# Kernel optimization log

Measured on AMD Instinct MI355X. Metric: run time of the kernel, lower is better.

Reference implementation:

```python
import jax, jax.numpy as jnp
import numpy as np

N, M, N0 = 100000, 12, 2500            # atoms, max neighbors, crystals
ORIG, C, NBR, H, NCONV = 92, 64, 41, 128, 3
EPS = 1e-5                              # torch BatchNorm1d default eps


def setup_inputs() -> dict:
    key = jax.random.key(0)
    ks = jax.random.split(key, 10)
    return {
        "atom_fea": jax.random.normal(ks[0], (N, ORIG), jnp.float32),
        "nbr_fea": jax.random.normal(ks[1], (N, M, NBR), jnp.float32),
        "nbr_fea_idx": jax.random.randint(ks[2], (N, M), 0, N),
        "crystal_atom_idx": jnp.sort(jax.random.randint(ks[3], (N,), 0, N0)),
        # learned parameters (Linear weights stored as (in, out))
        "emb_W": jax.random.normal(ks[4], (ORIG, C), jnp.float32) * 0.05,
        "emb_b": jnp.zeros((C,), jnp.float32),
        "fc_W": jax.random.normal(ks[5], (NCONV, 2 * C + NBR, 2 * C), jnp.float32) * 0.05,
        "fc_b": jnp.zeros((NCONV, 2 * C), jnp.float32),
        "bn1_g": jnp.ones((NCONV, 2 * C), jnp.float32),
        "bn1_b": jnp.zeros((NCONV, 2 * C), jnp.float32),
        "bn2_g": jnp.ones((NCONV, C), jnp.float32),
        "bn2_b": jnp.zeros((NCONV, C), jnp.float32),
        "head_W": jax.random.normal(ks[6], (C, H), jnp.float32) * 0.05,
        "head_b": jnp.zeros((H,), jnp.float32),
        "out_W": jax.random.normal(ks[7], (H, 1), jnp.float32) * 0.05,
        "out_b": jnp.zeros((1,), jnp.float32),
    }


def _bn(x, g, b):
    # training-mode BatchNorm1d: per-feature batch mean/var (biased)
    mu = jnp.mean(x, axis=0)
    var = jnp.var(x, axis=0)
    return (x - mu) * jax.lax.rsqrt(var + EPS) * g + b


def reference(atom_fea, nbr_fea, nbr_fea_idx, crystal_atom_idx,
              emb_W, emb_b, fc_W, fc_b, bn1_g, bn1_b, bn2_g, bn2_b,
              head_W, head_b, out_W, out_b):
    h = atom_fea @ emb_W + emb_b                       # (N, C)
    for l in range(NCONV):
        nbr_h = h[nbr_fea_idx]                         # gather (N, M, C)
        self_h = jnp.broadcast_to(h[:, None, :], (N, M, C))
        tot = jnp.concatenate([self_h, nbr_h, nbr_fea], axis=2)  # (N, M, 2C+NBR)
        g = tot @ fc_W[l] + fc_b[l]                    # (N, M, 2C)
        g = _bn(g.reshape(-1, 2 * C), bn1_g[l], bn1_b[l]).reshape(N, M, 2 * C)
        filt = jax.nn.sigmoid(g[..., :C])
        core = jax.nn.softplus(g[..., C:])
        summed = jnp.sum(filt * core, axis=1)          # (N, C)
        summed = _bn(summed, bn2_g[l], bn2_b[l])
        h = jax.nn.softplus(h + summed)                # residual
    # per-crystal mean pooling via segment sum
    counts = jax.ops.segment_sum(jnp.ones((N,), h.dtype), crystal_atom_idx, num_segments=N0)
    crys = jax.ops.segment_sum(h, crystal_atom_idx, num_segments=N0) / jnp.maximum(counts, 1.0)[:, None]
    z = jax.nn.softplus(jax.nn.softplus(crys) @ head_W + head_b)  # (N0, H)
    return z @ out_W + out_b                            # (N0, 1)
```

## Files before the change

### kernel.cpp

```cpp
#include <hip/hip_runtime.h>

#define NA 100000
#define MN 12
#define KE 41
#define N0C 2500
#define EPSBN 1e-5f
#define ROWDW 24
#define CONV_BLOCKS 1024
#define CONV_WAVES (CONV_BLOCKS * 4)

typedef _Float16 h2v __attribute__((ext_vector_type(2)));
typedef _Float16 h8v __attribute__((ext_vector_type(8)));
typedef float f4v __attribute__((ext_vector_type(4)));
typedef unsigned int uint;
union H2U { uint u; h2v h; };

__device__ __forceinline__ float softplusf(float x){
  float e = __expf(-fabsf(x));
  return fmaxf(x, 0.f) + __logf(1.f + e);
}
__device__ __forceinline__ float sigmoidf(float x){
  return __fdividef(1.f, 1.f + __expf(-x));
}
__device__ __forceinline__ int waveid(){
  return __builtin_amdgcn_readfirstlane((int)((blockIdx.x * blockDim.x + threadIdx.x) >> 6));
}

__global__ __launch_bounds__(256) void k_cast_e(const float* __restrict__ e,
                                                uint* __restrict__ EF)
{
  const int TOT = NA * MN * ROWDW;
  for (int i = blockIdx.x * 256 + threadIdx.x; i < TOT; i += gridDim.x * 256) {
    int r = i / ROWDW, k2 = i - r * ROWDW;
    const float* row = e + (size_t)r * KE;
    float a = 0.f, b = 0.f;
    if (k2 < 20) { a = row[2 * k2]; b = row[2 * k2 + 1]; }
    else if (k2 == 20) { a = row[40]; }
    H2U cv; cv.h = h2v{(_Float16)a, (_Float16)b};
    EF[i] = cv.u;
  }
}

__global__ __launch_bounds__(256) void k_embed(const float* __restrict__ af,
                                               const float* __restrict__ W,
                                               const float* __restrict__ b,
                                               float* __restrict__ h, int nw)
{
  int t = threadIdx.x & 63;
  int wid = waveid();
  float bias = b[t];
  for (int n0 = wid * 2; n0 < NA; n0 += nw * 2) {
    int n1 = n0 + 1;
    bool has1 = (n1 < NA);
    const float* a0 = af + (size_t)n0 * 92;
    const float* a1 = af + (size_t)(has1 ? n1 : n0) * 92;
    float acc0 = bias, acc1 = bias;
#pragma unroll 4
    for (int k = 0; k < 92; ++k) {
      float w = W[k * 64 + t];
      acc0 += a0[k] * w;
      acc1 += a1[k] * w;
    }
    h[(size_t)n0 * 64 + t] = acc0;
    if (has1) h[(size_t)n1 * 64 + t] = acc1;
  }
}

__global__ __launch_bounds__(256) void k_hw(const float* __restrict__ h,
                                            const float* __restrict__ fcW,
                                            uint* __restrict__ hWs,
                                            uint* __restrict__ hWn, int nw)
{
  __shared__ float Wl[64 * 256];
  for (int i = threadIdx.x; i < 64 * 256; i += 256) {
    int c = i >> 8, q = i & 255;
    int j = q & 63, part = q >> 6;
    Wl[(c * 64 + j) * 4 + part] = fcW[(c + ((part >> 1) << 6)) * 128 + ((part & 1) << 6) + j];
  }
  __syncthreads();
  int t = threadIdx.x & 63;
  int wid = waveid();
  const float4* W4 = (const float4*)Wl;
  for (int n0 = wid * 2; n0 < NA; n0 += nw * 2) {
    int n1 = n0 + 1;
    bool has1 = (n1 < NA);
    const float* ha = h + (size_t)n0 * 64;
    const float* hb = h + (size_t)(has1 ? n1 : n0) * 64;
    float4 A = {0,0,0,0}, B = {0,0,0,0};
#pragma unroll 4
    for (int c = 0; c < 64; ++c) {
      float4 w = W4[c * 64 + t];
      float x0 = ha[c], x1 = hb[c];
      A.x += x0 * w.x; A.y += x0 * w.y; A.z += x0 * w.z; A.w += x0 * w.w;
      B.x += x1 * w.x; B.y += x1 * w.y; B.z += x1 * w.z; B.w += x1 * w.w;
    }
    H2U p0, p1;
    p0.h = h2v{(_Float16)A.x, (_Float16)A.y};
    p1.h = h2v{(_Float16)A.z, (_Float16)A.w};
    hWs[(size_t)n0 * 64 + t] = p0.u;
    hWn[(size_t)n0 * 64 + t] = p1.u;
    if (has1) {
      p0.h = h2v{(_Float16)B.x, (_Float16)B.y};
      p1.h = h2v{(_Float16)B.z, (_Float16)B.w};
      hWs[(size_t)n1 * 64 + t] = p0.u;
      hWn[(size_t)n1 * 64 + t] = p1.u;
    }
  }
}

template<int APPLY>
__global__ __launch_bounds__(256) void k_conv(const uint* __restrict__ EF,
                                              const uint* __restrict__ hWs,
                                              const uint* __restrict__ hWn,
                                              const int*  __restrict__ idx,
                                              const float* __restrict__ We,
                                              const float* __restrict__ scsh,
                                              float* __restrict__ summed,
                                              float* __restrict__ stats)
{
  __shared__ float gt_all[4][16 * 132];
  int l = threadIdx.x & 63;
  int w = threadIdx.x >> 6;
  float* gt = gt_all[w];
  int wid = __builtin_amdgcn_readfirstlane(blockIdx.x * 4 + w);
  int c16 = l & 15, kg = l >> 4;

  h8v b1[8], b2[8];
#pragma unroll
  for (int T = 0; T < 8; ++T) {
    h8v v1 = {0,0,0,0,0,0,0,0}, v2 = {0,0,0,0,0,0,0,0};
#pragma unroll
    for (int j = 0; j < 8; ++j)
      v1[j] = (_Float16)We[(kg * 8 + j) * 128 + T * 16 + c16];
    if (kg < 2) {
#pragma unroll
      for (int j = 0; j < 8; ++j) {
        int k = 32 + kg * 8 + j;
        v2[j] = (k < KE) ? (_Float16)We[k * 128 + T * 16 + c16] : (_Float16)0.f;
      }
    }
    b1[T] = v1; b2[T] = v2;
  }

  float sc0 = 0, sh0 = 0, sc1 = 0, sh1 = 0;
  if (APPLY) { sc0 = scsh[l]; sc1 = scsh[l + 64]; sh0 = scsh[128 + l]; sh1 = scsh[192 + l]; }
  float s0 = 0, q0 = 0, s1 = 0, q1 = 0;

  for (int n = wid; n < NA; n += CONV_WAVES) {
    const uint* ep = EF + (size_t)n * (MN * ROWDW);
    h8v a1 = {0,0,0,0,0,0,0,0}, a2 = {0,0,0,0,0,0,0,0};
    if (c16 < MN) {
      a1 = *(const h8v*)(ep + c16 * ROWDW + kg * 4);
      if (kg < 2) a2 = *(const h8v*)(ep + c16 * ROWDW + 16 + kg * 4);
    }
    f4v acc[8];
#pragma unroll
    for (int T = 0; T < 8; ++T) acc[T] = f4v{0.f, 0.f, 0.f, 0.f};
#pragma unroll
    for (int T = 0; T < 8; ++T)
      acc[T] = __builtin_amdgcn_mfma_f32_16x16x32_f16(a1, b1[T], acc[T], 0, 0, 0);
#pragma unroll
    for (int T = 0; T < 8; ++T)
      acc[T] = __builtin_amdgcn_mfma_f32_16x16x32_f16(a2, b2[T], acc[T], 0, 0, 0);

#pragma unroll
    for (int T = 0; T < 8; ++T)
#pragma unroll
      for (int r = 0; r < 4; ++r)
        gt[(kg * 4 + r) * 132 + T * 16 + c16] = acc[T][r];

    const int* ip = idx + n * MN;
    H2U sp; sp.u = hWs[(size_t)n * 64 + l];
    float self0 = (float)sp.h[0], self1 = (float)sp.h[1];
    uint nbp[MN];
#pragma unroll
    for (int m = 0; m < MN; ++m) nbp[m] = hWn[(size_t)ip[m] * 64 + l];
    float accsum = 0.f;
#pragma unroll
    for (int m = 0; m < MN; ++m) {
      H2U nv; nv.u = nbp[m];
      float g0 = gt[m * 132 + l]      + self0 + (float)nv.h[0];
      float g1 = gt[m * 132 + 64 + l] + self1 + (float)nv.h[1];
      if (APPLY) {
        float f  = sigmoidf(g0 * sc0 + sh0);
        float cr = softplusf(g1 * sc1 + sh1);
        accsum += f * cr;
      } else {
        s0 += g0; q0 += g0 * g0;
        s1 += g1; q1 += g1 * g1;
      }
    }
    if (APPLY) {
      summed[(size_t)n * 64 + l] = accsum;
      s0 += accsum; q0 += accsum * accsum;
    }
  }
  if (APPLY) {
    atomicAdd(&stats[l], s0);
    atomicAdd(&stats[64 + l], q0);
  } else {
    atomicAdd(&stats[l], s0);
    atomicAdd(&stats[64 + l], s1);
    atomicAdd(&stats[128 + l], q0);
    atomicAdd(&stats[192 + l], q1);
  }
}

__global__ void k_fin1(const float* __restrict__ st, const float* __restrict__ g,
                       const float* __restrict__ b, float* __restrict__ scsh)
{
  int j = threadIdx.x;
  float inv = 1.f / (float)(NA * MN);
  float mean = st[j] * inv;
  float var  = st[128 + j] * inv - mean * mean;
  float rstd = rsqrtf(var + EPSBN);
  float sc = g[j] * rstd;
  scsh[j] = sc;
  scsh[128 + j] = b[j] - mean * sc;
}
__global__ void k_fin2(const float* __restrict__ st, const float* __restrict__ g,
                       const float* __restrict__ b, float* __restrict__ scsh)
{
  int j = threadIdx.x;
  float inv = 1.f / (float)NA;
  float mean = st[j] * inv;
  float var  = st[64 + j] * inv - mean * mean;
  float rstd = rsqrtf(var + EPSBN);
  float sc = g[j] * rstd;
  scsh[j] = sc;
  scsh[64 + j] = b[j] - mean * sc;
}

__global__ __launch_bounds__(256) void k_bn2res(float* __restrict__ h,
                                                const float* __restrict__ summed,
                                                const float* __restrict__ scsh)
{
  int tot = NA * 64 / 4;
  const float4* s4 = (const float4*)summed;
  float4* h4 = (float4*)h;
  for (int i = blockIdx.x * blockDim.x + threadIdx.x; i < tot; i += gridDim.x * blockDim.x) {
    int c4 = i & 15;
    float4 sc = ((const float4*)scsh)[c4];
    float4 sh = ((const float4*)(scsh + 64))[c4];
    float4 hv = h4[i], sv = s4[i];
    hv.x = softplusf(hv.x + sv.x * sc.x + sh.x);
    hv.y = softplusf(hv.y + sv.y * sc.y + sh.y);
    hv.z = softplusf(hv.z + sv.z * sc.z + sh.z);
    hv.w = softplusf(hv.w + sv.w * sc.w + sh.w);
    h4[i] = hv;
  }
}

__global__ __launch_bounds__(256) void k_pool(const float* __restrict__ h,
                                              const int* __restrict__ cidx,
                                              float* __restrict__ csum,
                                              float* __restrict__ ccnt, int nw)
{
  int t = threadIdx.x & 63;
  int wid = waveid();
  int chunk = (NA + nw - 1) / nw;
  int n0 = wid * chunk;
  int n1 = min(n0 + chunk, NA);
  if (n0 >= NA) return;
  float acc = 0.f, cacc = 0.f;
  int cur = -1;
  for (int n = n0; n < n1; ++n) {
    int ci = cidx[n];
    if (ci != cur) {
      if (cur >= 0) {
        atomicAdd(&csum[(size_t)cur * 64 + t], acc);
        if (t == 0) atomicAdd(&ccnt[cur], cacc);
      }
      cur = ci; acc = 0.f; cacc = 0.f;
    }
    acc += h[(size_t)n * 64 + t];
    cacc += 1.f;
  }
  if (cur >= 0) {
    atomicAdd(&csum[(size_t)cur * 64 + t], acc);
    if (t == 0) atomicAdd(&ccnt[cur], cacc);
  }
}

__global__ __launch_bounds__(256) void k_head(const float* __restrict__ csum,
                                              const float* __restrict__ ccnt,
                                              const float* __restrict__ Wh,
                                              const float* __restrict__ bh,
                                              const float* __restrict__ Wo,
                                              const float* __restrict__ bo,
                                              float* __restrict__ out)
{
  __shared__ float Wl[64 * 128];
  for (int i = threadIdx.x; i < 64 * 128; i += 256) Wl[i] = Wh[i];
  __syncthreads();
  int t = threadIdx.x & 63;
  int ci = blockIdx.x * 4 + (threadIdx.x >> 6);
  if (ci >= N0C) return;
  float cnt = fmaxf(ccnt[ci], 1.f);
  float x = softplusf(csum[(size_t)ci * 64 + t] / cnt);
  float acc0 = 0.f, acc1 = 0.f;
#pragma unroll 4
  for (int c = 0; c < 64; ++c) {
    float xc = __shfl(x, c, 64);
    acc0 += xc * Wl[c * 128 + t];
    acc1 += xc * Wl[c * 128 + 64 + t];
  }
  float z0 = softplusf(acc0 + bh[t]);
  float z1 = softplusf(acc1 + bh[64 + t]);
  float part = z0 * Wo[t] + z1 * Wo[64 + t];
#pragma unroll
  for (int s = 32; s >= 1; s >>= 1) part += __shfl_xor(part, s, 64);
  if (t == 0) out[ci] = part + bo[0];
}

extern "C" void kernel_launch(void* const* d_in, const int* in_sizes, int n_in,
                              void* d_out, int out_size, void* d_ws, size_t ws_size,
                              hipStream_t stream)
{
  const float* af    = (const float*)d_in[0];
  const float* nbr   = (const float*)d_in[1];
  const int*   nidx  = (const int*)d_in[2];
  const int*   cidx  = (const int*)d_in[3];
  const float* embW  = (const float*)d_in[4];
  const float* embB  = (const float*)d_in[5];
  const float* fcW   = (const float*)d_in[6];
  const float* bn1g  = (const float*)d_in[8];
  const float* bn1b  = (const float*)d_in[9];
  const float* bn2g  = (const float*)d_in[10];
  const float* bn2b  = (const float*)d_in[11];
  const float* headW = (const float*)d_in[12];
  const float* headB = (const float*)d_in[13];
  const float* outW  = (const float*)d_in[14];
  const float* outB  = (const float*)d_in[15];
  float* out = (float*)d_out;

  float* ws = (float*)d_ws;
  size_t off = 0;
  float* h      = ws + off; off += (size_t)NA * 64;
  uint*  hWs    = (uint*)(ws + off); off += (size_t)NA * 64;
  uint*  hWn    = (uint*)(ws + off); off += (size_t)NA * 64;
  uint*  EF     = (uint*)(ws + off); off += (size_t)NA * MN * ROWDW;
  float* summed = ws + off; off += (size_t)NA * 64;
  float* zr     = ws + off;
  float* stats1 = zr;
  float* stats2 = stats1 + 3 * 256;
  float* csum   = stats2 + 3 * 128;
  float* ccnt   = csum + (size_t)N0C * 64;
  size_t zcount = 3 * 256 + 3 * 128 + (size_t)N0C * 64 + N0C;
  float* scsh1  = ccnt + N0C;
  float* scsh2  = scsh1 + 3 * 256;

  hipMemsetAsync(zr, 0, zcount * sizeof(float), stream);

  k_cast_e<<<4096, 256, 0, stream>>>(nbr, EF);
  k_embed<<<512, 256, 0, stream>>>(af, embW, embB, h, 2048);

  for (int l = 0; l < 3; ++l) {
    const float* Wl = fcW + (size_t)l * 169 * 128;
    const float* We = Wl + 128 * 128;
    k_hw<<<512, 256, 0, stream>>>(h, Wl, hWs, hWn, 2048);
    k_conv<0><<<CONV_BLOCKS, 256, 0, stream>>>(EF, hWs, hWn, nidx, We, nullptr, nullptr,
                                               stats1 + l * 256);
    k_fin1<<<1, 128, 0, stream>>>(stats1 + l * 256, bn1g + l * 128, bn1b + l * 128,
                                  scsh1 + l * 256);
    k_conv<1><<<CONV_BLOCKS, 256, 0, stream>>>(EF, hWs, hWn, nidx, We, scsh1 + l * 256,
                                               summed, stats2 + l * 128);
    k_fin2<<<1, 64, 0, stream>>>(stats2 + l * 128, bn2g + l * 64, bn2b + l * 64,
                                 scsh2 + l * 128);
    k_bn2res<<<2048, 256, 0, stream>>>(h, summed, scsh2 + l * 128);
  }

  k_pool<<<512, 256, 0, stream>>>(h, cidx, csum, ccnt, 2048);
  k_head<<<625, 256, 0, stream>>>(csum, ccnt, headW, headB, outW, outB, out);
}
```

Before: 1.624 ms.

## Consume MFMA accumulators in registers instead of staging through LDS

The conv kernel no longer writes the 16x128 MFMA output tile to shared memory and re-reads it per lane. Each lane now works directly on its accumulator fragment (neighbor rows kg*4+r, columns T*16+c16) and gathers the matching self and neighbor hW values per fragment. Per-atom sums and BN statistics are reduced with cross-lane shuffles. The grid is doubled, since dropping LDS usage permits more resident blocks. The cost is more scattered gathers (4 dwords per neighbor per lane, 16 distinct loads), extra shuffles, and lanes with kg==3 sitting idle in the epilogue.

```diff
diff --git a/kernel.cpp b/kernel.cpp
--- a/kernel.cpp
+++ b/kernel.cpp
@@ -6,7 +6,7 @@
 #define N0C 2500
 #define EPSBN 1e-5f
 #define ROWDW 24
-#define CONV_BLOCKS 1024
+#define CONV_BLOCKS 2048
 #define CONV_WAVES (CONV_BLOCKS * 4)
 
 typedef _Float16 h2v __attribute__((ext_vector_type(2)));
@@ -118,10 +118,8 @@
                                               float* __restrict__ summed,
                                               float* __restrict__ stats)
 {
-  __shared__ float gt_all[4][16 * 132];
   int l = threadIdx.x & 63;
   int w = threadIdx.x >> 6;
-  float* gt = gt_all[w];
   int wid = __builtin_amdgcn_readfirstlane(blockIdx.x * 4 + w);
   int c16 = l & 15, kg = l >> 4;
 
@@ -142,9 +140,16 @@
     b1[T] = v1; b2[T] = v2;
   }
 
-  float sc0 = 0, sh0 = 0, sc1 = 0, sh1 = 0;
-  if (APPLY) { sc0 = scsh[l]; sc1 = scsh[l + 64]; sh0 = scsh[128 + l]; sh1 = scsh[192 + l]; }
-  float s0 = 0, q0 = 0, s1 = 0, q1 = 0;
+  float scT[8], shT[8];
+  if (APPLY) {
+#pragma unroll
+    for (int T = 0; T < 8; ++T) {
+      scT[T] = scsh[T * 16 + c16];
+      shT[T] = scsh[128 + T * 16 + c16];
+    }
+  }
+  float ss[8] = {0,0,0,0,0,0,0,0}, qq[8] = {0,0,0,0,0,0,0,0};
+  float bs[4] = {0,0,0,0}, bq[4] = {0,0,0,0};
 
   for (int n = wid; n < NA; n += CONV_WAVES) {
     const uint* ep = EF + (size_t)n * (MN * ROWDW);
@@ -163,46 +168,90 @@
     for (int T = 0; T < 8; ++T)
       acc[T] = __builtin_amdgcn_mfma_f32_16x16x32_f16(a2, b2[T], acc[T], 0, 0, 0);
 
-#pragma unroll
-    for (int T = 0; T < 8; ++T)
-#pragma unroll
-      for (int r = 0; r < 4; ++r)
-        gt[(kg * 4 + r) * 132 + T * 16 + c16] = acc[T][r];
-
+    float sf[8];
+#pragma unroll
+    for (int T = 0; T < 4; ++T) {
+      H2U sp; sp.u = hWs[(size_t)n * 64 + c16 + 16 * T];
+      sf[T] = (float)sp.h[0]; sf[T + 4] = (float)sp.h[1];
+    }
     const int* ip = idx + n * MN;
-    H2U sp; sp.u = hWs[(size_t)n * 64 + l];
-    float self0 = (float)sp.h[0], self1 = (float)sp.h[1];
-    uint nbp[MN];
-#pragma unroll
-    for (int m = 0; m < MN; ++m) nbp[m] = hWn[(size_t)ip[m] * 64 + l];
-    float accsum = 0.f;
-#pragma unroll
-    for (int m = 0; m < MN; ++m) {
-      H2U nv; nv.u = nbp[m];
-      float g0 = gt[m * 132 + l]      + self0 + (float)nv.h[0];
-      float g1 = gt[m * 132 + 64 + l] + self1 + (float)nv.h[1];
-      if (APPLY) {
-        float f  = sigmoidf(g0 * sc0 + sh0);
-        float cr = softplusf(g1 * sc1 + sh1);
-        accsum += f * cr;
-      } else {
-        s0 += g0; q0 += g0 * g0;
-        s1 += g1; q1 += g1 * g1;
-      }
-    }
-    if (APPLY) {
-      summed[(size_t)n * 64 + l] = accsum;
-      s0 += accsum; q0 += accsum * accsum;
-    }
-  }
-  if (APPLY) {
-    atomicAdd(&stats[l], s0);
-    atomicAdd(&stats[64 + l], q0);
+    uint nbp[4][4];
+    if (kg < 3) {
+#pragma unroll
+      for (int r = 0; r < 4; ++r) {
+        int nbi = ip[kg * 4 + r];
+#pragma unroll
+        for (int T = 0; T < 4; ++T)
+          nbp[r][T] = hWn[(size_t)nbi * 64 + c16 + 16 * T];
+      }
+    }
+
+    if (!APPLY) {
+      if (kg < 3) {
+#pragma unroll
+        for (int r = 0; r < 4; ++r)
+#pragma unroll
+          for (int T = 0; T < 4; ++T) {
+            H2U nv; nv.u = nbp[r][T];
+            float g0 = acc[T][r]     + sf[T]     + (float)nv.h[0];
+            float g1 = acc[T + 4][r] + sf[T + 4] + (float)nv.h[1];
+            ss[T] += g0;     qq[T] += g0 * g0;
+            ss[T + 4] += g1; qq[T + 4] += g1 * g1;
+          }
+      }
+    } else {
+      float accp[4] = {0.f, 0.f, 0.f, 0.f};
+      if (kg < 3) {
+#pragma unroll
+        for (int r = 0; r < 4; ++r)
+#pragma unroll
+          for (int T = 0; T < 4; ++T) {
+            H2U nv; nv.u = nbp[r][T];
+            float g0 = acc[T][r]     + sf[T]     + (float)nv.h[0];
+            float g1 = acc[T + 4][r] + sf[T + 4] + (float)nv.h[1];
+            float f  = sigmoidf(g0 * scT[T] + shT[T]);
+            float cr = softplusf(g1 * scT[T + 4] + shT[T + 4]);
+            accp[T] += f * cr;
+          }
+      }
+#pragma unroll
+      for (int T = 0; T < 4; ++T) {
+        accp[T] += __shfl_xor(accp[T], 16, 64);
+        accp[T] += __shfl_xor(accp[T], 32, 64);
+      }
+      if (kg == 0) {
+#pragma unroll
+        for (int T = 0; T < 4; ++T) {
+          summed[(size_t)n * 64 + T * 16 + c16] = accp[T];
+          bs[T] += accp[T]; bq[T] += accp[T] * accp[T];
+        }
+      }
+    }
+  }
+
+  if (!APPLY) {
+#pragma unroll
+    for (int T = 0; T < 8; ++T) {
+      ss[T] += __shfl_xor(ss[T], 16, 64);
+      ss[T] += __shfl_xor(ss[T], 32, 64);
+      qq[T] += __shfl_xor(qq[T], 16, 64);
+      qq[T] += __shfl_xor(qq[T], 32, 64);
+    }
+    if (kg == 0) {
+#pragma unroll
+      for (int T = 0; T < 8; ++T) {
+        atomicAdd(&stats[T * 16 + c16], ss[T]);
+        atomicAdd(&stats[128 + T * 16 + c16], qq[T]);
+      }
+    }
   } else {
-    atomicAdd(&stats[l], s0);
-    atomicAdd(&stats[64 + l], s1);
-    atomicAdd(&stats[128 + l], q0);
-    atomicAdd(&stats[192 + l], q1);
+    if (kg == 0) {
+#pragma unroll
+      for (int T = 0; T < 4; ++T) {
+        atomicAdd(&stats[T * 16 + c16], bs[T]);
+        atomicAdd(&stats[64 + T * 16 + c16], bq[T]);
+      }
+    }
   }
 }
 
@@ -359,8 +408,8 @@
     const float* Wl = fcW + (size_t)l * 169 * 128;
     const float* We = Wl + 128 * 128;
     k_hw<<<512, 256, 0, stream>>>(h, Wl, hWs, hWn, 2048);
-    k_conv<0><<<CONV_BLOCKS, 256, 0, stream>>>(EF, hWs, hWn, nidx, We, nullptr, nullptr,
-                                               stats1 + l * 256);
+    k_conv<0><<<CONV_BLOCKS, 256, 0, stream>>>(EF, hWs, hWn, nidx, We, nullptr,
+                                               nullptr, stats1 + l * 256);
     k_fin1<<<1, 128, 0, stream>>>(stats1 + l * 256, bn1g + l * 128, bn1b + l * 128,
                                   scsh1 + l * 256);
     k_conv<1><<<CONV_BLOCKS, 256, 0, stream>>>(EF, hWs, hWn, nidx, We, scsh1 + l * 256,
```

Result: slower. 2.094 ms (+28.9%).
